# Optimization experiments

Measured on AMD Instinct MI355X. Metric: run time of the kernel, lower is better.

Reference implementation:

```python
import jax, jax.numpy as jnp
import numpy as np

HEADS = 12
EPS = 1e-12  # torch F.normalize eps


def _l2_normalize(x, axis):
    norm = jnp.sqrt(jnp.sum(x * x, axis=axis, keepdims=True))
    return x / jnp.maximum(norm, EPS)


def setup_inputs() -> dict:
    key = jax.random.key(0)
    k1, k2, k3 = jax.random.split(key, 3)
    B, N, D = 8, 4096, 768
    x = jax.random.normal(k1, (B, N, D), dtype=jnp.float32)
    Wqkv = jax.random.normal(k2, (D, 3 * D), dtype=jnp.float32) * (1.0 / np.sqrt(D))
    temperature = jnp.ones((1, HEADS, 1, 1), dtype=jnp.float32)
    Wout = jax.random.normal(k3, (D, D), dtype=jnp.float32) * (1.0 / np.sqrt(D))
    bout = jnp.zeros((D,), dtype=jnp.float32)
    return {"x": x, "Wqkv": Wqkv, "temperature": temperature, "Wout": Wout, "bout": bout}


def reference(x, Wqkv, temperature, Wout, bout):
    B, N, D = x.shape
    H = HEADS
    d = D // H
    qkv = x @ Wqkv  # (B, N, 3D)
    q, k, v = jnp.split(qkv, 3, axis=-1)
    # b n (h d) -> b h n d
    def to_bhnd(t):
        return t.reshape(B, N, H, d).transpose(0, 2, 1, 3)
    q = to_bhnd(q)
    k = to_bhnd(k)
    v = to_bhnd(v)
    # q: normalize over token axis (torch: q is bhnd, dim=-2 -> n)
    q = _l2_normalize(q, axis=2)
    # k: torch layout is bhdn, normalized over dim=-1 (n); in bhnd that's axis=2
    k = _l2_normalize(k, axis=2) * temperature  # (1,H,1,1) broadcasts over bhnd
    # attention[p, q_idx] = sum_n k[n, p] * q[n, q_idx]  -> (B, H, d, d)
    attn = jnp.einsum('bhnp,bhnq->bhpq', k, q)
    attn = jax.nn.softmax(attn, axis=-1)
    # out[n, q_idx] = sum_p v[n, p] * attn[p, q_idx]
    out = jnp.einsum('bhnp,bhpq->bhnq', v, attn)
    # b h n d -> b n (h d)
    out = out.transpose(0, 2, 1, 3).reshape(B, N, D)
    return out @ Wout + bout
```

## Files before the change

kernel.cpp:

```cpp
#include <hip/hip_runtime.h>

typedef __attribute__((ext_vector_type(8))) short short8;
typedef __attribute__((ext_vector_type(4))) float f32x4;

__device__ __forceinline__ float b2f(unsigned short u) {
    unsigned int i = ((unsigned int)u) << 16;
    return __builtin_bit_cast(float, i);
}
__device__ __forceinline__ unsigned short f2b(float f) {
    unsigned int u = __builtin_bit_cast(unsigned int, f);
    unsigned int r = (u + 0x7fffu + ((u >> 16) & 1u)) >> 16;
    return (unsigned short)r;
}

__device__ __forceinline__ void async16(unsigned short* lds, const unsigned short* g) {
    __builtin_amdgcn_global_load_lds(
        (const __attribute__((address_space(1))) unsigned int*)g,
        (__attribute__((address_space(3))) unsigned int*)lds,
        16, 0, 0);
}

__device__ __forceinline__ void xcd_swizzle(int& bx, int& by) {
    if ((gridDim.y & 7) == 0) {
        const int nx = gridDim.x;
        const int rows_per_xcd = gridDim.y >> 3;
        const int flat = blockIdx.y * nx + blockIdx.x;
        const int xcd = flat & 7;
        const int i = flat >> 3;
        by = xcd * rows_per_xcd + i / nx;
        bx = i % nx;
    } else {
        bx = blockIdx.x; by = blockIdx.y;
    }
}

__global__ __launch_bounds__(256)
void cvt_f32_bf16(const float* __restrict__ in, unsigned short* __restrict__ out,
                  long long n8) {
    const long long i = ((long long)blockIdx.x * 256 + threadIdx.x) * 8;
    if (i >= n8) return;
    f32x4 a = *(const f32x4*)(in + i);
    f32x4 b = *(const f32x4*)(in + i + 4);
    short8 o;
    #pragma unroll
    for (int j = 0; j < 4; ++j) { o[j] = (short)f2b(a[j]); o[j + 4] = (short)f2b(b[j]); }
    *(short8*)(out + i) = o;
}

__global__ __launch_bounds__(256)
void transpose_f32_bf16(const float* __restrict__ in, unsigned short* __restrict__ out,
                        int R, int C) {
    __shared__ unsigned short t[32][33];
    const int r0 = blockIdx.y * 32, c0 = blockIdx.x * 32;
    const int tx = threadIdx.x & 31, ty = threadIdx.x >> 5;
    #pragma unroll
    for (int i = 0; i < 32; i += 8)
        t[ty + i][tx] = f2b(in[(size_t)(r0 + ty + i) * C + c0 + tx]);
    __syncthreads();
    #pragma unroll
    for (int i = 0; i < 32; i += 8)
        out[(size_t)(c0 + ty + i) * R + r0 + tx] = t[tx][ty + i];
}

__global__ __launch_bounds__(256)
void cvt_tr(const float* __restrict__ in, unsigned short* __restrict__ rm,
            unsigned short* __restrict__ tm) {
    __shared__ unsigned short t[32][33];
    const int r0 = blockIdx.y * 32, c0 = blockIdx.x * 32;
    const int tx = threadIdx.x & 31, ty = threadIdx.x >> 5;
    #pragma unroll
    for (int i = 0; i < 32; i += 8) {
        unsigned short v = f2b(in[(size_t)(r0 + ty + i) * 768 + c0 + tx]);
        t[ty + i][tx] = v;
        rm[(size_t)(r0 + ty + i) * 768 + c0 + tx] = v;
    }
    __syncthreads();
    #pragma unroll
    for (int i = 0; i < 32; i += 8)
        tm[(size_t)(c0 + ty + i) * 32768 + r0 + tx] = t[tx][ty + i];
}

template<int OM>
__global__ __launch_bounds__(256, 2)
void gemm_bt_g(const unsigned short* A, const unsigned short* BT,
               void* __restrict__ Cv, const float* __restrict__ bias,
               int K, int lda, int ldb, int ldc,
               long long sA, long long sB, long long sC) {
    __shared__ unsigned short As[128 * 32];
    __shared__ unsigned short Bs[128 * 32];
    const int z = blockIdx.z;
    A  += (size_t)z * sA;
    BT += (size_t)z * sB;
    int bxi, byi;
    xcd_swizzle(bxi, byi);
    const int tid  = threadIdx.x;
    const int wave = tid >> 6, lane = tid & 63;
    const int quad = lane >> 4, m16 = lane & 15;
    const int bm = byi * 128, bn = bxi * 128;
    const int wm = (wave >> 1) * 64, wn = (wave & 1) * 64;
    const int srow = wave * 32 + (lane >> 2);
    const int scol = (lane & 3) * 8;
    const unsigned short* Ag = A + (size_t)(bm + srow) * lda + scol;
    const unsigned short* Bg = BT + (size_t)(bn + srow) * ldb + scol;
    unsigned short* Asw = &As[(wave * 32) * 32];
    unsigned short* Bsw = &Bs[(wave * 32) * 32];
    f32x4 acc[4][4] = {};

    for (int k0 = 0; k0 < K; k0 += 32) {
        __syncthreads();
        async16(Asw,           Ag + k0);
        async16(Asw + 16 * 32, Ag + k0 + (size_t)16 * lda);
        async16(Bsw,           Bg + k0);
        async16(Bsw + 16 * 32, Bg + k0 + (size_t)16 * ldb);
        __syncthreads();
        short8 af[4], bfr[4];
        #pragma unroll
        for (int i = 0; i < 4; ++i)
            af[i] = *(const short8*)&As[(wm + i * 16 + m16) * 32 + quad * 8];
        #pragma unroll
        for (int j = 0; j < 4; ++j)
            bfr[j] = *(const short8*)&Bs[(wn + j * 16 + m16) * 32 + quad * 8];
        #pragma unroll
        for (int i = 0; i < 4; ++i)
            #pragma unroll
            for (int j = 0; j < 4; ++j)
                acc[i][j] = __builtin_amdgcn_mfma_f32_16x16x32_bf16(af[i], bfr[j], acc[i][j], 0, 0, 0);
    }

    if constexpr (OM == 0) {
        unsigned short* C = (unsigned short*)Cv + (size_t)z * sC;
        #pragma unroll
        for (int j = 0; j < 4; ++j) {
            const int col = bn + wn + j * 16 + m16;
            #pragma unroll
            for (int i = 0; i < 4; ++i)
                #pragma unroll
                for (int r = 0; r < 4; ++r) {
                    const int row = bm + wm + i * 16 + quad * 4 + r;
                    C[(size_t)row * ldc + col] = f2b(acc[i][j][r]);
                }
        }
    } else {
        float* C = (float*)Cv + (size_t)z * sC;
        #pragma unroll
        for (int j = 0; j < 4; ++j) {
            const int col = bn + wn + j * 16 + m16;
            const float bv = (OM == 2) ? bias[col] : 0.0f;
            #pragma unroll
            for (int i = 0; i < 4; ++i)
                #pragma unroll
                for (int r = 0; r < 4; ++r) {
                    const int row = bm + wm + i * 16 + quad * 4 + r;
                    C[(size_t)row * ldc + col] = acc[i][j][r] + bv;
                }
        }
    }
}

__global__ __launch_bounds__(256)
void rownorm(const unsigned short* __restrict__ W, const unsigned short* __restrict__ T,
             float* __restrict__ qn2, float* __restrict__ kn2) {
    const int row = blockIdx.x * 4 + (threadIdx.x >> 6);
    const int lane = threadIdx.x & 63;
    const int b = row / 1536, j = row % 1536;
    const unsigned short* wr = W + (size_t)j * 768;
    const unsigned short* tr = T + (size_t)b * 1179648 + (size_t)j * 768;
    float s = 0.f;
    {
        short8 a = *(const short8*)(wr + lane * 8);
        short8 c = *(const short8*)(tr + lane * 8);
        #pragma unroll
        for (int e = 0; e < 8; ++e) s += b2f((unsigned short)a[e]) * b2f((unsigned short)c[e]);
    }
    if (lane < 32) {
        short8 a = *(const short8*)(wr + 512 + lane * 8);
        short8 c = *(const short8*)(tr + 512 + lane * 8);
        #pragma unroll
        for (int e = 0; e < 8; ++e) s += b2f((unsigned short)a[e]) * b2f((unsigned short)c[e]);
    }
    #pragma unroll
    for (int o = 32; o; o >>= 1) s += __shfl_down(s, o);
    if (lane == 0) {
        if (j < 768) qn2[b * 768 + j] = s;
        else         kn2[b * 768 + j - 768] = s;
    }
}

__global__ __launch_bounds__(64)
void softmax_attn(const float* __restrict__ S, const float* __restrict__ qn2,
                  const float* __restrict__ kn2, const float* __restrict__ temp,
                  unsigned short* __restrict__ BTat) {
    const int bh = blockIdx.x, b = bh / 12, h = bh % 12, p = threadIdx.x;
    const float t = temp[h];
    const float knv = fmaxf(sqrtf(kn2[b * 768 + h * 64 + p]), 1e-12f);
    const float* Sr = S + (size_t)b * 589824 + (size_t)(h * 64 + p) * 768 + h * 64;
    const float* qr = qn2 + b * 768 + h * 64;
    float l[64];
    float mx = -1e30f;
    #pragma unroll
    for (int q = 0; q < 64; ++q) {
        const float qnv = fmaxf(sqrtf(qr[q]), 1e-12f);
        l[q] = t * Sr[q] / (knv * qnv);
        mx = fmaxf(mx, l[q]);
    }
    float sum = 0.f;
    #pragma unroll
    for (int q = 0; q < 64; ++q) { l[q] = __expf(l[q] - mx); sum += l[q]; }
    const float inv = 1.0f / sum;
    unsigned short* At = BTat + (size_t)b * 589824 + (size_t)(h * 64) * 768 + h * 64 + p;
    #pragma unroll
    for (int q = 0; q < 64; ++q) At[(size_t)q * 768] = f2b(l[q] * inv);
}

extern "C" void kernel_launch(void* const* d_in, const int* in_sizes, int n_in,
                              void* d_out, int out_size, void* d_ws, size_t ws_size,
                              hipStream_t stream) {
    const float *x = nullptr, *Wqkv = nullptr, *temp = nullptr, *Wout = nullptr, *bout = nullptr;
    for (int i = 0; i < n_in; ++i) {
        switch (in_sizes[i]) {
            case 25165824: x    = (const float*)d_in[i]; break;
            case 1769472:  Wqkv = (const float*)d_in[i]; break;
            case 12:       temp = (const float*)d_in[i]; break;
            case 589824:   Wout = (const float*)d_in[i]; break;
            case 768:      bout = (const float*)d_in[i]; break;
        }
    }
    float* out = (float*)d_out;

    char* ws = (char*)d_ws;
    unsigned short* WqkvT = (unsigned short*)(ws + 0);
    unsigned short* WoutT = (unsigned short*)(ws + 3538944);
    unsigned short* Wbf   = (unsigned short*)(ws + 4718592);
    unsigned short* xb    = (unsigned short*)(ws + 8257536);
    unsigned short* xT    = (unsigned short*)(ws + 58589184);
    unsigned short* TQKT  = (unsigned short*)(ws + 58589184);
    float*          Sfull = (float*)         (ws + 77463552);
    float*          qn2   = (float*)         (ws + 96337920);
    float*          kn2   = (float*)         (ws + 96362496);
    unsigned short* G     = (unsigned short*)(ws + 108920832);
    unsigned short* BTat  = (unsigned short*)(ws + 118358016);
    unsigned short* W2    = (unsigned short*)(ws + 127795200);
    unsigned short* FT    = (unsigned short*)(ws + 137232384);
    (void)ws_size;

    transpose_f32_bf16<<<dim3(2304 / 32, 768 / 32), 256, 0, stream>>>(Wqkv, WqkvT, 768, 2304);
    transpose_f32_bf16<<<dim3(768 / 32, 768 / 32), 256, 0, stream>>>(Wout, WoutT, 768, 768);
    cvt_f32_bf16<<<dim3(864), 256, 0, stream>>>(Wqkv, Wbf, 1769472LL);
    hipMemsetAsync(BTat, 0, 9437184, stream);

    cvt_tr<<<dim3(24, 1024), 256, 0, stream>>>(x, xb, xT);

    gemm_bt_g<0><<<dim3(6, 6, 8), 256, 0, stream>>>(
        xT, xT, G, nullptr, 4096, 32768, 32768, 768, 4096LL, 4096LL, 589824LL);

    gemm_bt_g<0><<<dim3(6, 12, 8), 256, 0, stream>>>(
        WqkvT, G, TQKT, nullptr, 768, 768, 768, 768, 0LL, 589824LL, 1179648LL);

    rownorm<<<dim3(3072), 256, 0, stream>>>(WqkvT, TQKT, qn2, kn2);

    gemm_bt_g<1><<<dim3(6, 6, 8), 256, 0, stream>>>(
        WqkvT + 589824, TQKT, Sfull, nullptr, 768, 768, 768, 768, 0LL, 1179648LL, 589824LL);

    softmax_attn<<<dim3(96), 64, 0, stream>>>(Sfull, qn2, kn2, temp, BTat);

    gemm_bt_g<0><<<dim3(6, 6, 8), 256, 0, stream>>>(
        Wbf + 1536, BTat, W2, nullptr, 768, 2304, 768, 768, 0LL, 589824LL, 589824LL);

    gemm_bt_g<0><<<dim3(6, 6, 8), 256, 0, stream>>>(
        WoutT, W2, FT, nullptr, 768, 768, 768, 768, 0LL, 589824LL, 589824LL);

    gemm_bt_g<2><<<dim3(6, 32, 8), 256, 0, stream>>>(
        xb, FT, out, bout, 768, 768, 768, 768, 3145728LL, 589824LL, 3145728LL);
}
```

Before: 449.4 us.

## Split-K Gram GEMM, fuse per-head scores/softmax/value GEMM, vectorize x transpose

The 4096-deep Gram GEMM x^T x is split over four K-chunks (4x more blocks) and reduced by a separate kernel, raising parallelism from 288 blocks. The dense full-size S GEMM, the softmax and the block-diagonal attention GEMM are replaced by one per-(batch,head) kernel that computes only the 64x64 diagonal score block, applies the softmax in shared memory and multiplies by the head's Wv slice directly. This removes wasted off-diagonal work, a memset and intermediate buffers. The x conversion/transpose now uses 64x64 tiles with vector loads and stores. The split-K partials are stored in bf16 before summing, which adds rounding error.

```diff
diff --git a/kernel.cpp b/kernel.cpp
--- a/kernel.cpp
+++ b/kernel.cpp
@@ -63,21 +63,110 @@
 }
 
 __global__ __launch_bounds__(256)
-void cvt_tr(const float* __restrict__ in, unsigned short* __restrict__ rm,
-            unsigned short* __restrict__ tm) {
-    __shared__ unsigned short t[32][33];
-    const int r0 = blockIdx.y * 32, c0 = blockIdx.x * 32;
-    const int tx = threadIdx.x & 31, ty = threadIdx.x >> 5;
-    #pragma unroll
-    for (int i = 0; i < 32; i += 8) {
-        unsigned short v = f2b(in[(size_t)(r0 + ty + i) * 768 + c0 + tx]);
-        t[ty + i][tx] = v;
-        rm[(size_t)(r0 + ty + i) * 768 + c0 + tx] = v;
-    }
-    __syncthreads();
-    #pragma unroll
-    for (int i = 0; i < 32; i += 8)
-        tm[(size_t)(c0 + ty + i) * 32768 + r0 + tx] = t[tx][ty + i];
+void cvt_tr64(const float* __restrict__ in, unsigned short* __restrict__ rm,
+              unsigned short* __restrict__ tm) {
+    __shared__ unsigned short T[64][72];
+    const int c0 = blockIdx.x * 64, r0 = blockIdx.y * 64;
+    const int tr = threadIdx.x >> 2, tc = (threadIdx.x & 3) * 16;
+    {
+        const float* src = in + (size_t)(r0 + tr) * 768 + c0 + tc;
+        f32x4 a0 = *(const f32x4*)(src);
+        f32x4 a1 = *(const f32x4*)(src + 4);
+        f32x4 a2 = *(const f32x4*)(src + 8);
+        f32x4 a3 = *(const f32x4*)(src + 12);
+        short8 o0, o1;
+        #pragma unroll
+        for (int j = 0; j < 4; ++j) {
+            o0[j] = (short)f2b(a0[j]); o0[j + 4] = (short)f2b(a1[j]);
+            o1[j] = (short)f2b(a2[j]); o1[j + 4] = (short)f2b(a3[j]);
+        }
+        *(short8*)&T[tr][tc] = o0;
+        *(short8*)&T[tr][tc + 8] = o1;
+        unsigned short* d = rm + (size_t)(r0 + tr) * 768 + c0 + tc;
+        *(short8*)(d) = o0;
+        *(short8*)(d + 8) = o1;
+    }
+    __syncthreads();
+    short8 s0, s1;
+    #pragma unroll
+    for (int e = 0; e < 8; ++e) {
+        s0[e] = (short)T[tc + e][tr];
+        s1[e] = (short)T[tc + 8 + e][tr];
+    }
+    unsigned short* d = tm + (size_t)(c0 + tr) * 32768 + r0 + tc;
+    *(short8*)(d) = s0;
+    *(short8*)(d + 8) = s1;
+}
+
+__global__ __launch_bounds__(256, 2)
+void gram_split(const unsigned short* __restrict__ xT, unsigned short* __restrict__ Gp) {
+    __shared__ unsigned short As[128 * 32];
+    __shared__ unsigned short Bs[128 * 32];
+    const int z = blockIdx.z, b = z >> 2, s = z & 3;
+    const int tid  = threadIdx.x;
+    const int wave = tid >> 6, lane = tid & 63;
+    const int quad = lane >> 4, m16 = lane & 15;
+    const int bm = blockIdx.y * 128, bn = blockIdx.x * 128;
+    const int wm = (wave >> 1) * 64, wn = (wave & 1) * 64;
+    const int srow = wave * 32 + (lane >> 2);
+    const int scol = (lane & 3) * 8;
+    const unsigned short* base = xT + (size_t)b * 4096 + s * 1024 + scol;
+    const unsigned short* Ag = base + (size_t)(bm + srow) * 32768;
+    const unsigned short* Bg = base + (size_t)(bn + srow) * 32768;
+    unsigned short* Asw = &As[(wave * 32) * 32];
+    unsigned short* Bsw = &Bs[(wave * 32) * 32];
+    f32x4 acc[4][4] = {};
+
+    for (int k0 = 0; k0 < 1024; k0 += 32) {
+        __syncthreads();
+        async16(Asw,           Ag + k0);
+        async16(Asw + 16 * 32, Ag + k0 + (size_t)16 * 32768);
+        async16(Bsw,           Bg + k0);
+        async16(Bsw + 16 * 32, Bg + k0 + (size_t)16 * 32768);
+        __syncthreads();
+        short8 af[4], bfr[4];
+        #pragma unroll
+        for (int i = 0; i < 4; ++i)
+            af[i] = *(const short8*)&As[(wm + i * 16 + m16) * 32 + quad * 8];
+        #pragma unroll
+        for (int j = 0; j < 4; ++j)
+            bfr[j] = *(const short8*)&Bs[(wn + j * 16 + m16) * 32 + quad * 8];
+        #pragma unroll
+        for (int i = 0; i < 4; ++i)
+            #pragma unroll
+            for (int j = 0; j < 4; ++j)
+                acc[i][j] = __builtin_amdgcn_mfma_f32_16x16x32_bf16(af[i], bfr[j], acc[i][j], 0, 0, 0);
+    }
+    unsigned short* C = Gp + (size_t)z * 589824;
+    #pragma unroll
+    for (int j = 0; j < 4; ++j) {
+        const int col = bn + wn + j * 16 + m16;
+        #pragma unroll
+        for (int i = 0; i < 4; ++i)
+            #pragma unroll
+            for (int r = 0; r < 4; ++r) {
+                const int row = bm + wm + i * 16 + quad * 4 + r;
+                C[(size_t)row * 768 + col] = f2b(acc[i][j][r]);
+            }
+    }
+}
+
+__global__ __launch_bounds__(256)
+void g_reduce(const unsigned short* __restrict__ Gp, unsigned short* __restrict__ G) {
+    const int b = blockIdx.y;
+    const int off = blockIdx.x * 2048 + threadIdx.x * 8;
+    const unsigned short* p = Gp + (size_t)b * 4 * 589824 + off;
+    float s[8] = {};
+    #pragma unroll
+    for (int sp = 0; sp < 4; ++sp) {
+        short8 v = *(const short8*)(p + (size_t)sp * 589824);
+        #pragma unroll
+        for (int e = 0; e < 8; ++e) s[e] += b2f((unsigned short)v[e]);
+    }
+    short8 o;
+    #pragma unroll
+    for (int e = 0; e < 8; ++e) o[e] = (short)f2b(s[e]);
+    *(short8*)(G + (size_t)b * 589824 + off) = o;
 }
 
 template<int OM>
@@ -145,7 +234,7 @@
         #pragma unroll
         for (int j = 0; j < 4; ++j) {
             const int col = bn + wn + j * 16 + m16;
-            const float bv = (OM == 2) ? bias[col] : 0.0f;
+            const float bv = bias[col];
             #pragma unroll
             for (int i = 0; i < 4; ++i)
                 #pragma unroll
@@ -186,30 +275,113 @@
     }
 }
 
-__global__ __launch_bounds__(64)
-void softmax_attn(const float* __restrict__ S, const float* __restrict__ qn2,
-                  const float* __restrict__ kn2, const float* __restrict__ temp,
-                  unsigned short* __restrict__ BTat) {
-    const int bh = blockIdx.x, b = bh / 12, h = bh % 12, p = threadIdx.x;
-    const float t = temp[h];
-    const float knv = fmaxf(sqrtf(kn2[b * 768 + h * 64 + p]), 1e-12f);
-    const float* Sr = S + (size_t)b * 589824 + (size_t)(h * 64 + p) * 768 + h * 64;
-    const float* qr = qn2 + b * 768 + h * 64;
-    float l[64];
-    float mx = -1e30f;
-    #pragma unroll
-    for (int q = 0; q < 64; ++q) {
-        const float qnv = fmaxf(sqrtf(qr[q]), 1e-12f);
-        l[q] = t * Sr[q] / (knv * qnv);
-        mx = fmaxf(mx, l[q]);
-    }
+__global__ __launch_bounds__(256)
+void head_fused(const unsigned short* __restrict__ WqkvT,
+                const unsigned short* __restrict__ TQKT,
+                const unsigned short* __restrict__ Wbf,
+                const float* __restrict__ qn2, const float* __restrict__ kn2,
+                const float* __restrict__ temp, unsigned short* __restrict__ W2) {
+    const int bh = blockIdx.x, b = bh / 12, h = bh % 12;
+    __shared__ unsigned short As[64][72], Bs[64][72], At[64][72];
+    __shared__ float Sf[64][65];
+    __shared__ float qinv[64], kinv[64], red[64][4], red2[64][4];
+    const int tid = threadIdx.x;
+    const int wave = tid >> 6, lane = tid & 63;
+    const int quad = lane >> 4, m16 = lane & 15;
+    const int wr = wave >> 1, wc = wave & 1;
+
+    if (tid < 64) {
+        qinv[tid] = 1.0f / fmaxf(sqrtf(qn2[b * 768 + h * 64 + tid]), 1e-12f);
+        kinv[tid] = 1.0f / fmaxf(sqrtf(kn2[b * 768 + h * 64 + tid]), 1e-12f);
+    }
+
+    f32x4 sacc[2][2] = {};
+    const int srow = tid >> 3, scol8 = (tid & 7) * 8;
+    const unsigned short* Arow = WqkvT + (size_t)(768 + h * 64) * 768;
+    const unsigned short* Brow = TQKT + (size_t)(b * 1536 + h * 64) * 768;
+    for (int k0 = 0; k0 < 768; k0 += 64) {
+        __syncthreads();
+        *(short8*)&As[srow][scol8]      = *(const short8*)(Arow + (size_t)srow * 768 + k0 + scol8);
+        *(short8*)&As[srow + 32][scol8] = *(const short8*)(Arow + (size_t)(srow + 32) * 768 + k0 + scol8);
+        *(short8*)&Bs[srow][scol8]      = *(const short8*)(Brow + (size_t)srow * 768 + k0 + scol8);
+        *(short8*)&Bs[srow + 32][scol8] = *(const short8*)(Brow + (size_t)(srow + 32) * 768 + k0 + scol8);
+        __syncthreads();
+        #pragma unroll
+        for (int ks = 0; ks < 2; ++ks) {
+            short8 af[2], bv[2];
+            af[0] = *(const short8*)&As[wr * 32 + m16][ks * 32 + quad * 8];
+            af[1] = *(const short8*)&As[wr * 32 + 16 + m16][ks * 32 + quad * 8];
+            bv[0] = *(const short8*)&Bs[wc * 32 + m16][ks * 32 + quad * 8];
+            bv[1] = *(const short8*)&Bs[wc * 32 + 16 + m16][ks * 32 + quad * 8];
+            #pragma unroll
+            for (int i = 0; i < 2; ++i)
+                #pragma unroll
+                for (int j = 0; j < 2; ++j)
+                    sacc[i][j] = __builtin_amdgcn_mfma_f32_16x16x32_bf16(af[i], bv[j], sacc[i][j], 0, 0, 0);
+        }
+    }
+    __syncthreads();
+    #pragma unroll
+    for (int i = 0; i < 2; ++i)
+        #pragma unroll
+        for (int j = 0; j < 2; ++j)
+            #pragma unroll
+            for (int r = 0; r < 4; ++r)
+                Sf[wr * 32 + i * 16 + quad * 4 + r][wc * 32 + j * 16 + m16] = sacc[i][j][r];
+    __syncthreads();
+
+    const float tt = temp[h];
+    const int p = tid & 63, g = tid >> 6;
+    float l[16], mx = -1e30f;
+    const float kvp = tt * kinv[p];
+    #pragma unroll
+    for (int e = 0; e < 16; ++e) {
+        l[e] = kvp * Sf[p][g * 16 + e] * qinv[g * 16 + e];
+        mx = fmaxf(mx, l[e]);
+    }
+    red[p][g] = mx;
+    __syncthreads();
+    mx = fmaxf(fmaxf(red[p][0], red[p][1]), fmaxf(red[p][2], red[p][3]));
     float sum = 0.f;
     #pragma unroll
-    for (int q = 0; q < 64; ++q) { l[q] = __expf(l[q] - mx); sum += l[q]; }
+    for (int e = 0; e < 16; ++e) { l[e] = __expf(l[e] - mx); sum += l[e]; }
+    red2[p][g] = sum;
+    __syncthreads();
+    sum = red2[p][0] + red2[p][1] + red2[p][2] + red2[p][3];
     const float inv = 1.0f / sum;
-    unsigned short* At = BTat + (size_t)b * 589824 + (size_t)(h * 64) * 768 + h * 64 + p;
-    #pragma unroll
-    for (int q = 0; q < 64; ++q) At[(size_t)q * 768] = f2b(l[q] * inv);
+    #pragma unroll
+    for (int e = 0; e < 16; ++e) At[g * 16 + e][p] = f2b(l[e] * inv);
+    __syncthreads();
+
+    const unsigned short* Wv = Wbf + 1536 + h * 64;
+    unsigned short* W2b = W2 + (size_t)b * 589824 + h * 64;
+    #pragma unroll
+    for (int pass = 0; pass < 3; ++pass) {
+        const int rb = wave * 192 + pass * 64;
+        f32x4 wacc[4][4] = {};
+        #pragma unroll
+        for (int ks = 0; ks < 2; ++ks) {
+            short8 av[4], bv[4];
+            #pragma unroll
+            for (int i = 0; i < 4; ++i)
+                av[i] = *(const short8*)(Wv + (size_t)(rb + i * 16 + m16) * 2304 + ks * 32 + quad * 8);
+            #pragma unroll
+            for (int j = 0; j < 4; ++j)
+                bv[j] = *(const short8*)&At[j * 16 + m16][ks * 32 + quad * 8];
+            #pragma unroll
+            for (int i = 0; i < 4; ++i)
+                #pragma unroll
+                for (int j = 0; j < 4; ++j)
+                    wacc[i][j] = __builtin_amdgcn_mfma_f32_16x16x32_bf16(av[i], bv[j], wacc[i][j], 0, 0, 0);
+        }
+        #pragma unroll
+        for (int j = 0; j < 4; ++j)
+            #pragma unroll
+            for (int i = 0; i < 4; ++i)
+                #pragma unroll
+                for (int r = 0; r < 4; ++r)
+                    W2b[(size_t)(rb + i * 16 + quad * 4 + r) * 768 + j * 16 + m16] = f2b(wacc[i][j][r]);
+    }
 }
 
 extern "C" void kernel_launch(void* const* d_in, const int* in_sizes, int n_in,
@@ -233,38 +405,30 @@
     unsigned short* Wbf   = (unsigned short*)(ws + 4718592);
     unsigned short* xb    = (unsigned short*)(ws + 8257536);
     unsigned short* xT    = (unsigned short*)(ws + 58589184);
-    unsigned short* TQKT  = (unsigned short*)(ws + 58589184);
-    float*          Sfull = (float*)         (ws + 77463552);
-    float*          qn2   = (float*)         (ws + 96337920);
-    float*          kn2   = (float*)         (ws + 96362496);
-    unsigned short* G     = (unsigned short*)(ws + 108920832);
-    unsigned short* BTat  = (unsigned short*)(ws + 118358016);
-    unsigned short* W2    = (unsigned short*)(ws + 127795200);
-    unsigned short* FT    = (unsigned short*)(ws + 137232384);
+    unsigned short* G     = (unsigned short*)(ws + 58589184);
+    unsigned short* TQKT  = (unsigned short*)(ws + 68026368);
+    float*          qn2   = (float*)         (ws + 86900736);
+    float*          kn2   = (float*)         (ws + 86925312);
+    unsigned short* W2    = (unsigned short*)(ws + 86949888);
+    unsigned short* FT    = (unsigned short*)(ws + 96387072);
+    unsigned short* Gp    = (unsigned short*)(ws + 108920832);
     (void)ws_size;
 
-    transpose_f32_bf16<<<dim3(2304 / 32, 768 / 32), 256, 0, stream>>>(Wqkv, WqkvT, 768, 2304);
-    transpose_f32_bf16<<<dim3(768 / 32, 768 / 32), 256, 0, stream>>>(Wout, WoutT, 768, 768);
+    transpose_f32_bf16<<<dim3(72, 24), 256, 0, stream>>>(Wqkv, WqkvT, 768, 2304);
+    transpose_f32_bf16<<<dim3(24, 24), 256, 0, stream>>>(Wout, WoutT, 768, 768);
     cvt_f32_bf16<<<dim3(864), 256, 0, stream>>>(Wqkv, Wbf, 1769472LL);
-    hipMemsetAsync(BTat, 0, 9437184, stream);
-
-    cvt_tr<<<dim3(24, 1024), 256, 0, stream>>>(x, xb, xT);
-
-    gemm_bt_g<0><<<dim3(6, 6, 8), 256, 0, stream>>>(
-        xT, xT, G, nullptr, 4096, 32768, 32768, 768, 4096LL, 4096LL, 589824LL);
+
+    cvt_tr64<<<dim3(12, 512), 256, 0, stream>>>(x, xb, xT);
+
+    gram_split<<<dim3(6, 6, 32), 256, 0, stream>>>(xT, Gp);
+    g_reduce<<<dim3(288, 8), 256, 0, stream>>>(Gp, G);
 
     gemm_bt_g<0><<<dim3(6, 12, 8), 256, 0, stream>>>(
         WqkvT, G, TQKT, nullptr, 768, 768, 768, 768, 0LL, 589824LL, 1179648LL);
 
     rownorm<<<dim3(3072), 256, 0, stream>>>(WqkvT, TQKT, qn2, kn2);
 
-    gemm_bt_g<1><<<dim3(6, 6, 8), 256, 0, stream>>>(
-        WqkvT + 589824, TQKT, Sfull, nullptr, 768, 768, 768, 768, 0LL, 1179648LL, 589824LL);
-
-    softmax_attn<<<dim3(96), 64, 0, stream>>>(Sfull, qn2, kn2, temp, BTat);
-
-    gemm_bt_g<0><<<dim3(6, 6, 8), 256, 0, stream>>>(
-        Wbf + 1536, BTat, W2, nullptr, 768, 2304, 768, 768, 0LL, 589824LL, 589824LL);
+    head_fused<<<dim3(96), 256, 0, stream>>>(WqkvT, TQKT, Wbf, qn2, kn2, temp, W2);
 
     gemm_bt_g<0><<<dim3(6, 6, 8), 256, 0, stream>>>(
         WoutT, W2, FT, nullptr, 768, 768, 768, 768, 0LL, 589824LL, 589824LL);
```

Result: faster. 424.0 us (-5.7%).
